# Kernel tuning notes

Measured on AMD Instinct MI355X. Metric: run time of the kernel, lower is better.

The kernel has to match this reference:

```python
import jax, jax.numpy as jnp
import numpy as np

HEAD_SIZE = 64


def setup_inputs() -> dict:
    key = jax.random.key(0)
    ks = jax.random.split(key, 10)
    B, S, D, H, hs = 4, 2048, 768, 12, HEAD_SIZE
    F = 4 * D
    sd = lambda n: 1.0 / np.sqrt(n)
    return {
        "x": jax.random.normal(ks[0], (B, S, D), jnp.float32),
        "Wq": jax.random.normal(ks[1], (H, D, hs), jnp.float32) * sd(D),
        "Wk": jax.random.normal(ks[2], (H, D, hs), jnp.float32) * sd(D),
        "Wv": jax.random.normal(ks[3], (H, D, hs), jnp.float32) * sd(D),
        "Wo": jax.random.normal(ks[4], (D, D), jnp.float32) * sd(D),
        "bo": jnp.zeros((D,), jnp.float32),
        "W1": jax.random.normal(ks[5], (D, F), jnp.float32) * sd(D),
        "b1": jnp.zeros((F,), jnp.float32),
        "W2": jax.random.normal(ks[6], (F, D), jnp.float32) * sd(F),
        "b2": jnp.zeros((D,), jnp.float32),
    }


def reference(x, Wq, Wk, Wv, Wo, bo, W1, b1, W2, b2):
    B, S, D = x.shape
    hs = Wq.shape[-1]
    # per-head projections (no bias), vectorized over heads: [B,H,S,hs]
    q = jnp.einsum("bsd,hde->bhse", x, Wq)
    k = jnp.einsum("bsd,hde->bhse", x, Wk)
    v = jnp.einsum("bsd,hde->bhse", x, Wv)
    # causal attention scores [B,H,S,S], scaled by sqrt(head_size)
    scores = jnp.einsum("bhse,bhte->bhst", q, k) / jnp.sqrt(jnp.float32(hs))
    causal = jnp.tril(jnp.ones((S, S), dtype=bool))
    scores = jnp.where(causal, scores, -jnp.inf)
    attn = jax.nn.softmax(scores, axis=-1)
    z = jnp.einsum("bhst,bhte->bhse", attn, v)
    # concat heads along feature dim (head order preserved) -> [B,S,D]
    z = z.transpose(0, 2, 1, 3).reshape(B, S, D)
    # output projection + residual
    z = z @ Wo + bo + x
    # FFN + residual
    h = jax.nn.relu(z @ W1 + b1)
    return h @ W2 + b2 + z
```

## Files before the change

kernel.cpp:

```cpp
#include <hip/hip_runtime.h>


typedef __attribute__((ext_vector_type(4))) float f32x4;
typedef __attribute__((ext_vector_type(8))) short bf16x8;
typedef __attribute__((ext_vector_type(4))) unsigned short u16x4;

#define GLB_AS __attribute__((address_space(1)))
#define LDS_AS __attribute__((address_space(3)))

__device__ __forceinline__ unsigned short f2bf(float f) {
  unsigned int u = __float_as_uint(f);
  u = (u + 0x7FFFu + ((u >> 16) & 1u)) >> 16;
  return (unsigned short)u;
}

__device__ __forceinline__ void gload16(const void* g, void* l) {
  __builtin_amdgcn_global_load_lds((const GLB_AS unsigned int*)g,
                                   (LDS_AS unsigned int*)l, 16, 0, 0);
}

__device__ __forceinline__ int xcd_swz(int orig, int nwg) {
  int q = nwg >> 3, r = nwg & 7;
  int xcd = orig & 7, rest = orig >> 3;
  return (xcd < r ? xcd * (q + 1) : r * (q + 1) + (xcd - r) * q) + rest;
}

__global__ void castx(const float* __restrict__ in, unsigned short* __restrict__ out, int n) {
  int i = (blockIdx.x * 256 + threadIdx.x) * 4;
  if (i < n) {
    float4 f = *(const float4*)&in[i];
    u16x4 o;
    o[0] = f2bf(f.x); o[1] = f2bf(f.y); o[2] = f2bf(f.z); o[3] = f2bf(f.w);
    *(u16x4*)&out[i] = o;
  }
}

__global__ void reduce2(const float* __restrict__ p, float* __restrict__ out, int n) {
  int i = (blockIdx.x * 256 + threadIdx.x) * 4;
  if (i < n) {
    f32x4 a = *(const f32x4*)&p[i];
    f32x4 b = *(const f32x4*)&p[n + i];
    a += b;
    *(f32x4*)&out[i] = a;
  }
}

__global__ void tcast(const float* __restrict__ in, unsigned short* __restrict__ out,
                      int R, int C, float scale) {
  __shared__ float tile[32][33];
  const float* inb = in + (size_t)blockIdx.z * R * C;
  unsigned short* outb = out + (size_t)blockIdx.z * R * C;
  int bx = blockIdx.x * 32;
  int by = blockIdx.y * 32;
  int tx = threadIdx.x, ty = threadIdx.y;
  #pragma unroll
  for (int i = 0; i < 32; i += 8)
    tile[ty + i][tx] = inb[(size_t)(by + ty + i) * C + bx + tx];
  __syncthreads();
  #pragma unroll
  for (int i = 0; i < 32; i += 8)
    outb[(size_t)(bx + ty + i) * R + by + tx] = f2bf(tile[tx][ty + i] * scale);
}

__global__ void tcast3(const float* __restrict__ Wq, const float* __restrict__ Wk,
                       const float* __restrict__ Wv, unsigned short* __restrict__ out,
                       float qscale) {
  __shared__ float tile[32][33];
  const int R = 768, C = 64;
  int z = blockIdx.z, wsel = z / 12, head = z % 12;
  const float* in = (wsel == 0 ? Wq : wsel == 1 ? Wk : Wv) + (size_t)head * R * C;
  unsigned short* outb = out + (size_t)wsel * R * R + (size_t)head * R * C;
  float scale = wsel == 0 ? qscale : 1.0f;
  int bx = blockIdx.x * 32;
  int by = blockIdx.y * 32;
  int tx = threadIdx.x, ty = threadIdx.y;
  #pragma unroll
  for (int i = 0; i < 32; i += 8)
    tile[ty + i][tx] = in[(size_t)(by + ty + i) * C + bx + tx];
  __syncthreads();
  #pragma unroll
  for (int i = 0; i < 32; i += 8)
    outb[(size_t)(bx + ty + i) * R + by + tx] = f2bf(tile[tx][ty + i] * scale);
}

__global__ void vtrans(const unsigned short* __restrict__ v, unsigned short* __restrict__ vT) {
  __shared__ unsigned short tile[32][33];
  int bh = blockIdx.z, b = bh / 12, h = bh % 12;
  int s0 = blockIdx.x * 32, e0 = blockIdx.y * 32;
  int tx = threadIdx.x, ty = threadIdx.y;
  #pragma unroll
  for (int i = 0; i < 32; i += 8)
    tile[ty + i][tx] = v[(size_t)(b * 2048 + s0 + ty + i) * 768 + h * 64 + e0 + tx];
  __syncthreads();
  #pragma unroll
  for (int i = 0; i < 32; i += 8)
    vT[(size_t)((b * 12 + h) * 64 + e0 + ty + i) * 2048 + s0 + tx] = tile[tx][ty + i];
}

template <int EPI>
__global__ void gemm_bf16(const unsigned short* __restrict__ A,
                          const unsigned short* __restrict__ Bt,
                          const float* __restrict__ bias,
                          const float* __restrict__ resid,
                          float* __restrict__ Cf,
                          unsigned short* __restrict__ Cb,
                          int M, int N, int K, int gy, size_t segN) {
  __shared__ unsigned short Alds[2][128 * 32];
  __shared__ unsigned short Blds[2][128 * 32];
  const int tid = threadIdx.x;
  const int lane = tid & 63;
  const int w = tid >> 6;
  const int wm = w & 1, wn = w >> 1;
  const int wg = xcd_swz(blockIdx.x, gridDim.x);
  const int gsz = 8 * gy;
  const int group = wg / gsz;
  const int rem = wg - group * gsz;
  const int bm = (group * 8 + (rem & 7)) * 128;
  const int bn = (rem >> 3) * 128;

  f32x4 acc[4][4] = {};

  const int r0 = tid >> 2;
  const int c0 = (tid & 3) * 8;

  #pragma unroll
  for (int i = 0; i < 2; ++i) {
    int row = r0 + i * 64;
    gload16(&A[(size_t)(bm + row) * K + c0], &Alds[0][row * 32 + c0]);
    gload16(&Bt[(size_t)(bn + row) * K + c0], &Blds[0][row * 32 + c0]);
  }
  __syncthreads();

  int buf = 0;
  for (int k0 = 0; k0 < K; k0 += 32) {
    if (k0 + 32 < K) {
      #pragma unroll
      for (int i = 0; i < 2; ++i) {
        int row = r0 + i * 64;
        gload16(&A[(size_t)(bm + row) * K + k0 + 32 + c0], &Alds[buf ^ 1][row * 32 + c0]);
        gload16(&Bt[(size_t)(bn + row) * K + k0 + 32 + c0], &Blds[buf ^ 1][row * 32 + c0]);
      }
    }
    bf16x8 af[4], bf[4];
    #pragma unroll
    for (int m = 0; m < 4; ++m)
      af[m] = *(const bf16x8*)&Alds[buf][(wm * 64 + m * 16 + (lane & 15)) * 32 + (lane >> 4) * 8];
    #pragma unroll
    for (int n = 0; n < 4; ++n)
      bf[n] = *(const bf16x8*)&Blds[buf][(wn * 64 + n * 16 + (lane & 15)) * 32 + (lane >> 4) * 8];
    #pragma unroll
    for (int m = 0; m < 4; ++m)
      #pragma unroll
      for (int n = 0; n < 4; ++n)
        acc[m][n] = __builtin_amdgcn_mfma_f32_16x16x32_bf16(af[m], bf[n], acc[m][n], 0, 0, 0);
    __syncthreads();
    buf ^= 1;
  }

  const int crow0 = bm + wm * 64 + ((lane >> 4)) * 4;
  const int ccol0 = bn + wn * 64 + (lane & 15);
  #pragma unroll
  for (int m = 0; m < 4; ++m) {
    #pragma unroll
    for (int n = 0; n < 4; ++n) {
      int col = ccol0 + n * 16;
      #pragma unroll
      for (int r = 0; r < 4; ++r) {
        int row = crow0 + m * 16 + r;
        float v = acc[m][n][r];
        if constexpr (EPI & 1) v += bias[col];
        if constexpr (EPI & 4) v += resid[(size_t)row * N + col];
        if constexpr (EPI & 2) v = fmaxf(v, 0.f);
        if constexpr (EPI & 8) Cf[(size_t)row * N + col] = v;
        if constexpr (EPI & 16) Cb[(size_t)row * N + col] = f2bf(v);
      }
    }
  }
}


#define STG(b, X, h, kt) {                                                 \
    const unsigned short* _s = (X) ? Bt : A;                               \
    const int _rb = (X) ? bn : bm;                                         \
    _Pragma("unroll") for (int _l = 0; _l < 2; ++_l) {                     \
      int _r = (h) * 128 + _l * 64 + s_row;                                \
      gload16(&_s[(size_t)(_rb + _r) * K + kof + (kt) * 64 + s_gc8],       \
              &lds[b][X][_r * 64 + s_sc8]);                                \
    } }

#define VMW4 asm volatile("s_waitcnt vmcnt(4)" ::: "memory")
#define VMW0 asm volatile("s_waitcnt vmcnt(0)" ::: "memory")

#define PHASE(q, b, WITHB, STGSTMT, VMSTMT)                                 \
  {                                                                         \
    Af[0] = *(const bf16x8*)&lds[b][0][aBase + (2*(q)+0)*1024 + sc0];       \
    Af[1] = *(const bf16x8*)&lds[b][0][aBase + (2*(q)+0)*1024 + sc1];       \
    Af[2] = *(const bf16x8*)&lds[b][0][aBase + (2*(q)+1)*1024 + sc0];       \
    Af[3] = *(const bf16x8*)&lds[b][0][aBase + (2*(q)+1)*1024 + sc1];       \
    if (WITHB) {                                                            \
      _Pragma("unroll") for (int nf = 0; nf < 4; ++nf) {                    \
        Bf[nf*2+0] = *(const bf16x8*)&lds[b][1][bBase + nf*1024 + sc0];     \
        Bf[nf*2+1] = *(const bf16x8*)&lds[b][1][bBase + nf*1024 + sc1];     \
      }                                                                     \
    }                                                                       \
    STGSTMT;                                                                \
    __builtin_amdgcn_sched_barrier(0);                                      \
    __builtin_amdgcn_s_barrier();                                           \
    asm volatile("s_waitcnt lgkmcnt(0)" ::: "memory");                      \
    __builtin_amdgcn_sched_barrier(0);                                      \
    __builtin_amdgcn_s_setprio(1);                                          \
    _Pragma("unroll") for (int mi = 0; mi < 2; ++mi)                        \
      _Pragma("unroll") for (int nf = 0; nf < 4; ++nf) {                    \
        acc[2*(q)+mi][nf] = __builtin_amdgcn_mfma_f32_16x16x32_bf16(        \
            Af[mi*2+0], Bf[nf*2+0], acc[2*(q)+mi][nf], 0, 0, 0);            \
        acc[2*(q)+mi][nf] = __builtin_amdgcn_mfma_f32_16x16x32_bf16(        \
            Af[mi*2+1], Bf[nf*2+1], acc[2*(q)+mi][nf], 0, 0, 0);            \
      }                                                                     \
    __builtin_amdgcn_s_setprio(0);                                          \
    VMSTMT;                                                                 \
    __builtin_amdgcn_sched_barrier(0);                                      \
    __builtin_amdgcn_s_barrier();                                           \
  }

template <int EPI>
__global__ __launch_bounds__(512, 2)
void gemm256(const unsigned short* __restrict__ A,
             const unsigned short* __restrict__ Bt,
             const float* __restrict__ bias,
             const float* __restrict__ resid,
             float* __restrict__ Cf,
             unsigned short* __restrict__ Cb,
             int M, int N, int K, int gy, size_t segN) {
  __shared__ unsigned short lds[2][2][16384];
  const int tid = threadIdx.x;
  const int lane = tid & 63;
  const int w = tid >> 6;
  const int wr = w >> 2, wc = w & 3;
  const int q16 = lane & 15, qt = lane >> 4;

  int wg = xcd_swz(blockIdx.x, gridDim.x);
  int ks = 0;
  if constexpr ((EPI & 64) != 0) { ks = wg & 1; wg >>= 1; }
  const int gsz = 4 * gy;
  const int group = wg / gsz;
  const int rem = wg - group * gsz;
  const int bm = (group * 4 + (rem & 3)) * 256;
  const int bn = (rem >> 2) * 256;

  const int Kh  = (EPI & 64) ? (K >> 1) : K;
  const int kof = ks * Kh;

  const int s_row = tid >> 3;
  const int s_sc  = tid & 7;
  const int s_sc8 = s_sc * 8;
  const int s_gc8 = (s_sc ^ (s_row & 7)) * 8;

  const int aBase = (wr * 128 + q16) * 64;
  const int bBase = (wc * 64 + q16) * 64;
  const int sc0 = (qt ^ (q16 & 7)) * 8;
  const int sc1 = ((4 + qt) ^ (q16 & 7)) * 8;

  f32x4 acc[8][4] = {};
  bf16x8 Af[4], Bf[8];

  const int nt = Kh >> 6;

  STG(0, 0, 0, 0) STG(0, 0, 1, 0) STG(0, 1, 0, 0) STG(0, 1, 1, 0)
  STG(1, 1, 0, 1) STG(1, 1, 1, 1)
  VMW4;
  __builtin_amdgcn_s_barrier();

  for (int t = 0; t < nt; t += 2) {
    const bool s2 = t + 2 < nt, s3 = t + 3 < nt;
    PHASE(0, 0, true,  STG(1, 0, 0, t + 1),            (void)0)
    PHASE(1, 0, false, STG(1, 0, 1, t + 1),            (void)0)
    PHASE(2, 0, false, if (s2) STG(0, 1, 0, t + 2),    (void)0)
    PHASE(3, 0, false, if (s2) STG(0, 1, 1, t + 2),    if (s2) { VMW4; } else { VMW0; })
    PHASE(0, 1, true,  if (s2) STG(0, 0, 0, t + 2),    (void)0)
    PHASE(1, 1, false, if (s2) STG(0, 0, 1, t + 2),    (void)0)
    PHASE(2, 1, false, if (s3) STG(1, 1, 0, t + 3),    (void)0)
    PHASE(3, 1, false, if (s3) STG(1, 1, 1, t + 3),    if (s3) { VMW4; } else if (s2) { VMW0; })
  }

  const int crow0 = bm + wr * 128 + qt * 4;
  const int ccol0 = bn + wc * 64 + q16;
  const int seg = bn / 768;
  const int lcol0 = (bn % 768) + wc * 64 + q16;
  #pragma unroll
  for (int mf = 0; mf < 8; ++mf) {
    #pragma unroll
    for (int nf = 0; nf < 4; ++nf) {
      int col = ccol0 + nf * 16;
      #pragma unroll
      for (int j = 0; j < 4; ++j) {
        int row = crow0 + mf * 16 + j;
        float v = acc[mf][nf][j];
        if constexpr (EPI & 64) {
          if (ks == 0) v += bias[col] + resid[(size_t)row * N + col];
          Cf[(size_t)ks * segN + (size_t)row * N + col] = v;
        } else {
          if constexpr (EPI & 1) v += bias[col];
          if constexpr (EPI & 4) v += resid[(size_t)row * N + col];
          if constexpr (EPI & 2) v = fmaxf(v, 0.f);
          if constexpr (EPI & 8) Cf[(size_t)row * N + col] = v;
          if constexpr (EPI & 16) Cb[(size_t)row * N + col] = f2bf(v);
          if constexpr (EPI & 32)
            Cb[(size_t)seg * segN + (size_t)row * 768 + lcol0 + nf * 16] = f2bf(v);
        }
      }
    }
  }
}

__global__ void attn_fwd(const unsigned short* __restrict__ q,
                         const unsigned short* __restrict__ k,
                         const unsigned short* __restrict__ vT,
                         unsigned short* __restrict__ z) {
  __shared__ unsigned short Klds[2 * 2 * 64 * 32];
  __shared__ unsigned short Vlds[2 * 2 * 64 * 32];
  __shared__ unsigned short Plds[4 * 16 * 72];

  const int wgid = xcd_swz(blockIdx.x, gridDim.x);
  const int pi = wgid & 15;
  const int bh = wgid >> 4;
  const int b = bh / 12, h = bh % 12;
  const int tid = threadIdx.x, lane = tid & 63, w = tid >> 6;
  const int q16 = lane & 15;
  const int qt  = lane >> 4;
  const int rdc = ((qt ^ ((q16 >> 1) & 3)) * 8);

  const int srow = tid >> 2;
  const int sdc  = (tid & 3) * 8;
  const int sgc  = (((tid & 3) ^ ((srow >> 1) & 3)) * 8);
  const size_t kbase = (size_t)(b * 2048) * 768 + h * 64;
  const size_t vbase = (size_t)((b * 12 + h) * 64) * 2048;
  unsigned short* Pw = &Plds[w * 16 * 72];

  #pragma unroll 1
  for (int seg = 0; seg < 2; ++seg) {
    const int qb = seg == 0 ? pi : 31 - pi;
    const int q0 = qb * 64;
    const int nt = qb + 1;

    const int qrow = q0 + w * 16 + q16;
    const size_t qoff = (size_t)(b * 2048 + qrow) * 768 + h * 64 + qt * 8;
    bf16x8 qf0 = *(const bf16x8*)&q[qoff];
    bf16x8 qf1 = *(const bf16x8*)&q[qoff + 32];

    f32x4 accO[4] = {};
    float lrow = 0.f;

    #pragma unroll
    for (int i = 0; i < 2; ++i) {
      gload16(&k[kbase + (size_t)srow * 768 + i * 32 + sgc],
              &Klds[i * 2048 + srow * 32 + sdc]);
      gload16(&vT[vbase + (size_t)srow * 2048 + i * 32 + sgc],
              &Vlds[i * 2048 + srow * 32 + sdc]);
    }
    __syncthreads();

    int buf = 0;
    for (int t = 0; t < nt; ++t) {
      if (t + 1 < nt) {
        const int kv1 = (t + 1) * 64;
        const int bo = (buf ^ 1) * 4096;
        #pragma unroll
        for (int i = 0; i < 2; ++i) {
          gload16(&k[kbase + (size_t)(kv1 + srow) * 768 + i * 32 + sgc],
                  &Klds[bo + i * 2048 + srow * 32 + sdc]);
          gload16(&vT[vbase + (size_t)srow * 2048 + kv1 + i * 32 + sgc],
                  &Vlds[bo + i * 2048 + srow * 32 + sdc]);
        }
      }

      const int kv0 = t * 64;
      const int kb_ = buf * 4096;

      f32x4 s[4];
      __builtin_amdgcn_s_setprio(1);
      #pragma unroll
      for (int n = 0; n < 4; ++n) {
        bf16x8 kf0 = *(const bf16x8*)&Klds[kb_ + 0 * 2048 + (n * 16 + q16) * 32 + rdc];
        bf16x8 kf1 = *(const bf16x8*)&Klds[kb_ + 1 * 2048 + (n * 16 + q16) * 32 + rdc];
        f32x4 acc0 = {};
        acc0 = __builtin_amdgcn_mfma_f32_16x16x32_bf16(kf0, qf0, acc0, 0, 0, 0);
        s[n] = __builtin_amdgcn_mfma_f32_16x16x32_bf16(kf1, qf1, acc0, 0, 0, 0);
      }
      __builtin_amdgcn_s_setprio(0);

      if (t == nt - 1) {
        const int rowg = q0 + w * 16 + q16;
        #pragma unroll
        for (int n = 0; n < 4; ++n)
          #pragma unroll
          for (int r = 0; r < 4; ++r)
            if (kv0 + n * 16 + qt * 4 + r > rowg) s[n][r] = -3.0e38f;
      }

      #pragma unroll
      for (int n = 0; n < 4; ++n)
        #pragma unroll
        for (int r = 0; r < 4; ++r) { s[n][r] = exp2f(s[n][r]); lrow += s[n][r]; }

      #pragma unroll
      for (int n = 0; n < 4; ++n) {
        unsigned int lo, hi;
        asm("v_cvt_pk_bf16_f32 %0, %1, %2" : "=v"(lo) : "v"(s[n][0]), "v"(s[n][1]));
        asm("v_cvt_pk_bf16_f32 %0, %1, %2" : "=v"(hi) : "v"(s[n][2]), "v"(s[n][3]));
        uint2 pk; pk.x = lo; pk.y = hi;
        *(uint2*)&Pw[q16 * 72 + n * 16 + qt * 4] = pk;
      }

      __builtin_amdgcn_s_setprio(1);
      #pragma unroll
      for (int kk = 0; kk < 2; ++kk) {
        bf16x8 pf = *(const bf16x8*)&Pw[q16 * 72 + kk * 32 + qt * 8];
        #pragma unroll
        for (int n = 0; n < 4; ++n) {
          bf16x8 vf = *(const bf16x8*)&Vlds[kb_ + kk * 2048 + (n * 16 + q16) * 32 + rdc];
          accO[n] = __builtin_amdgcn_mfma_f32_16x16x32_bf16(pf, vf, accO[n], 0, 0, 0);
        }
      }
      __builtin_amdgcn_s_setprio(0);

      __syncthreads();
      buf ^= 1;
    }

    lrow += __shfl_xor(lrow, 16);
    lrow += __shfl_xor(lrow, 32);
    #pragma unroll
    for (int r = 0; r < 4; ++r) {
      float lr = __int_as_float(__builtin_amdgcn_ds_bpermute((qt * 4 + r) * 4,
                                                             __float_as_int(lrow)));
      float linv = 1.0f / lr;
      int rowg = q0 + w * 16 + qt * 4 + r;
      #pragma unroll
      for (int n = 0; n < 4; ++n)
        z[(size_t)(b * 2048 + rowg) * 768 + h * 64 + n * 16 + q16]
            = f2bf(accO[n][r] * linv);
    }
  }
}

extern "C" void kernel_launch(void* const* d_in, const int* in_sizes, int n_in,
                              void* d_out, int out_size, void* d_ws, size_t ws_size,
                              hipStream_t stream) {
  const float* x  = (const float*)d_in[0];
  const float* Wq = (const float*)d_in[1];
  const float* Wk = (const float*)d_in[2];
  const float* Wv = (const float*)d_in[3];
  const float* Wo = (const float*)d_in[4];
  const float* bo = (const float*)d_in[5];
  const float* W1 = (const float*)d_in[6];
  const float* b1 = (const float*)d_in[7];
  const float* W2 = (const float*)d_in[8];
  const float* b2 = (const float*)d_in[9];
  float* out = (float*)d_out;

  const int B = 4, S = 2048, D = 768, H = 12, hs = 64, F = 3072;
  const int M = B * S;
  const size_t MD = (size_t)M * D;

  unsigned short* xb   = (unsigned short*)d_ws;
  unsigned short* qb   = xb + MD;
  unsigned short* kb   = qb + MD;
  unsigned short* vb   = kb + MD;
  unsigned short* hbuf = xb;
  unsigned short* vT   = vb + MD;
  unsigned short* zb   = vT + MD;
  float*          z2f  = (float*)(zb + MD);
  unsigned short* z2b  = (unsigned short*)(z2f + MD);
  unsigned short* wqkvT= z2b + MD;
  unsigned short* woT  = wqkvT + 3 * (size_t)D * D;
  unsigned short* w1T  = woT + (size_t)D * D;
  unsigned short* w2T  = w1T + (size_t)D * F;
  float*          part = (float*)qb;

  dim3 tb(32, 8);

  castx<<<dim3((int)(MD / 4 / 256)), 256, 0, stream>>>(x, xb, (int)MD);

  const float QS = 0.125f * 1.4426950408889634f;
  tcast3<<<dim3(hs / 32, D / 32, 3 * H), tb, 0, stream>>>(Wq, Wk, Wv, wqkvT, QS);
  tcast<<<dim3(D / 32, D / 32, 1), tb, 0, stream>>>(Wo, woT, D, D, 1.0f);
  tcast<<<dim3(F / 32, D / 32, 1), tb, 0, stream>>>(W1, w1T, D, F, 1.0f);
  tcast<<<dim3(D / 32, F / 32, 1), tb, 0, stream>>>(W2, w2T, F, D, 1.0f);

  {
    int gy = 3 * D / 256;
    gemm256<32><<<dim3((M / 256) * gy), 512, 0, stream>>>(xb, wqkvT, nullptr, nullptr,
                                                          nullptr, qb, M, 3 * D, D, gy, MD);
  }

  vtrans<<<dim3(S / 32, hs / 32, B * H), tb, 0, stream>>>(vb, vT);

  attn_fwd<<<dim3((S / 128) * B * H), 256, 0, stream>>>(qb, kb, vT, zb);

  {
    int gy = D / 128;
    gemm_bf16<1 | 4 | 8 | 16><<<dim3(64 * gy), 256, 0, stream>>>(zb, woT, bo, x,
                                                                 z2f, z2b, M, D, D, gy, 0);
  }
  {
    int gy = F / 256;
    gemm256<1 | 2 | 16><<<dim3((M / 256) * gy), 512, 0, stream>>>(z2b, w1T, b1, nullptr,
                                                                  nullptr, hbuf, M, F, D, gy, 0);
  }
  {
    int gy = D / 256;
    gemm256<64><<<dim3(2 * (M / 256) * gy), 512, 0, stream>>>(hbuf, w2T, b2, z2f,
                                                              part, nullptr, M, D, F, gy, MD);
    reduce2<<<dim3((int)(MD / 4 / 256)), 256, 0, stream>>>(part, out, (int)MD);
  }
}
```

Baseline: 298.0 us.

## Restage GEMM A/B loads by quarter and interleave MFMA chains

Splits the GEMM staging macro into separate A and B loaders. A is now staged in row quarters matching the compute phases, with finer-grained vmcnt waits so each phase waits only for the data it needs. The MFMA inner loop is reordered so the two k-halves issue as independent chains, which removes back-to-back accumulator dependencies. The attention QK^T step also preloads all K fragments and interleaves its MFMAs. The tighter wait counts risk correctness or stalls if the vmcnt accounting is wrong.

Result: no change. 303.3 us (+1.8%).

```diff
diff --git a/kernel.cpp b/kernel.cpp
--- a/kernel.cpp
+++ b/kernel.cpp
@@ -179,17 +179,21 @@
 }
 
 
-#define STG(b, X, h, kt) {                                                 \
-    const unsigned short* _s = (X) ? Bt : A;                               \
-    const int _rb = (X) ? bn : bm;                                         \
+#define STGB(b, h, kt) {                                                   \
     _Pragma("unroll") for (int _l = 0; _l < 2; ++_l) {                     \
       int _r = (h) * 128 + _l * 64 + s_row;                                \
-      gload16(&_s[(size_t)(_rb + _r) * K + kof + (kt) * 64 + s_gc8],       \
-              &lds[b][X][_r * 64 + s_sc8]);                                \
+      gload16(&Bt[(size_t)(bn + _r) * K + kof + (kt) * 64 + s_gc8],        \
+              &lds[b][1][_r * 64 + s_sc8]);                                \
     } }
 
-#define VMW4 asm volatile("s_waitcnt vmcnt(4)" ::: "memory")
-#define VMW0 asm volatile("s_waitcnt vmcnt(0)" ::: "memory")
+#define STGA(b, qd, kt) {                                                  \
+    _Pragma("unroll") for (int _l = 0; _l < 2; ++_l) {                     \
+      int _r = (qd) * 64 + _l * 128 + s_row;                               \
+      gload16(&A[(size_t)(bm + _r) * K + kof + (kt) * 64 + s_gc8],         \
+              &lds[b][0][_r * 64 + s_sc8]);                                \
+    } }
+
+#define VMW(N) asm volatile("s_waitcnt vmcnt(" #N ")" ::: "memory")
 
 #define PHASE(q, b, WITHB, STGSTMT, VMSTMT)                                 \
   {                                                                         \
@@ -209,13 +213,11 @@
     asm volatile("s_waitcnt lgkmcnt(0)" ::: "memory");                      \
     __builtin_amdgcn_sched_barrier(0);                                      \
     __builtin_amdgcn_s_setprio(1);                                          \
-    _Pragma("unroll") for (int mi = 0; mi < 2; ++mi)                        \
-      _Pragma("unroll") for (int nf = 0; nf < 4; ++nf) {                    \
-        acc[2*(q)+mi][nf] = __builtin_amdgcn_mfma_f32_16x16x32_bf16(        \
-            Af[mi*2+0], Bf[nf*2+0], acc[2*(q)+mi][nf], 0, 0, 0);            \
-        acc[2*(q)+mi][nf] = __builtin_amdgcn_mfma_f32_16x16x32_bf16(        \
-            Af[mi*2+1], Bf[nf*2+1], acc[2*(q)+mi][nf], 0, 0, 0);            \
-      }                                                                     \
+    _Pragma("unroll") for (int kk = 0; kk < 2; ++kk)                        \
+      _Pragma("unroll") for (int mi = 0; mi < 2; ++mi)                      \
+        _Pragma("unroll") for (int nf = 0; nf < 4; ++nf)                    \
+          acc[2*(q)+mi][nf] = __builtin_amdgcn_mfma_f32_16x16x32_bf16(      \
+              Af[mi*2+kk], Bf[nf*2+kk], acc[2*(q)+mi][nf], 0, 0, 0);        \
     __builtin_amdgcn_s_setprio(0);                                          \
     VMSTMT;                                                                 \
     __builtin_amdgcn_sched_barrier(0);                                      \
@@ -265,21 +267,22 @@
 
   const int nt = Kh >> 6;
 
-  STG(0, 0, 0, 0) STG(0, 0, 1, 0) STG(0, 1, 0, 0) STG(0, 1, 1, 0)
-  STG(1, 1, 0, 1) STG(1, 1, 1, 1)
-  VMW4;
+  STGB(0, 0, 0) STGB(0, 1, 0) STGA(0, 0, 0) STGA(0, 1, 0)
+  STGB(1, 0, 1) STGB(1, 1, 1)
+  VMW(6);
   __builtin_amdgcn_s_barrier();
 
+  #pragma unroll 1
   for (int t = 0; t < nt; t += 2) {
-    const bool s2 = t + 2 < nt, s3 = t + 3 < nt;
-    PHASE(0, 0, true,  STG(1, 0, 0, t + 1),            (void)0)
-    PHASE(1, 0, false, STG(1, 0, 1, t + 1),            (void)0)
-    PHASE(2, 0, false, if (s2) STG(0, 1, 0, t + 2),    (void)0)
-    PHASE(3, 0, false, if (s2) STG(0, 1, 1, t + 2),    if (s2) { VMW4; } else { VMW0; })
-    PHASE(0, 1, true,  if (s2) STG(0, 0, 0, t + 2),    (void)0)
-    PHASE(1, 1, false, if (s2) STG(0, 0, 1, t + 2),    (void)0)
-    PHASE(2, 1, false, if (s3) STG(1, 1, 0, t + 3),    (void)0)
-    PHASE(3, 1, false, if (s3) STG(1, 1, 1, t + 3),    if (s3) { VMW4; } else if (s2) { VMW0; })
+    const bool s2 = t + 2 < nt;
+    PHASE(0, 0, true,  STGA(1, 0, t + 1),            (void)0)
+    PHASE(1, 0, false, STGA(1, 1, t + 1),            VMW(8))
+    PHASE(2, 0, false, if (s2) STGB(0, 0, t + 2),    (void)0)
+    PHASE(3, 0, false, if (s2) STGB(0, 1, t + 2),    if (s2) { VMW(6); } else { VMW(2); })
+    PHASE(0, 1, true,  if (s2) STGA(0, 0, t + 2),    (void)0)
+    PHASE(1, 1, false, if (s2) STGA(0, 1, t + 2),    if (s2) { VMW(8); } else { VMW(0); })
+    PHASE(2, 1, false, if (s2) STGB(1, 0, t + 3),    (void)0)
+    PHASE(3, 1, false, if (s2) STGB(1, 1, t + 3),    if (s2) { VMW(6); } else { VMW(0); })
   }
 
   const int crow0 = bm + wr * 128 + qt * 4;
@@ -376,16 +379,22 @@
       const int kv0 = t * 64;
       const int kb_ = buf * 4096;
 
+      bf16x8 kf0[4], kf1[4];
+      #pragma unroll
+      for (int n = 0; n < 4; ++n) {
+        kf0[n] = *(const bf16x8*)&Klds[kb_ + 0 * 2048 + (n * 16 + q16) * 32 + rdc];
+        kf1[n] = *(const bf16x8*)&Klds[kb_ + 1 * 2048 + (n * 16 + q16) * 32 + rdc];
+      }
       f32x4 s[4];
       __builtin_amdgcn_s_setprio(1);
       #pragma unroll
       for (int n = 0; n < 4; ++n) {
-        bf16x8 kf0 = *(const bf16x8*)&Klds[kb_ + 0 * 2048 + (n * 16 + q16) * 32 + rdc];
-        bf16x8 kf1 = *(const bf16x8*)&Klds[kb_ + 1 * 2048 + (n * 16 + q16) * 32 + rdc];
-        f32x4 acc0 = {};
-        acc0 = __builtin_amdgcn_mfma_f32_16x16x32_bf16(kf0, qf0, acc0, 0, 0, 0);
-        s[n] = __builtin_amdgcn_mfma_f32_16x16x32_bf16(kf1, qf1, acc0, 0, 0, 0);
-      }
+        f32x4 zz = {};
+        s[n] = __builtin_amdgcn_mfma_f32_16x16x32_bf16(kf0[n], qf0, zz, 0, 0, 0);
+      }
+      #pragma unroll
+      for (int n = 0; n < 4; ++n)
+        s[n] = __builtin_amdgcn_mfma_f32_16x16x32_bf16(kf1[n], qf1, s[n], 0, 0, 0);
       __builtin_amdgcn_s_setprio(0);
 
       if (t == nt - 1) {
```
